# Performance work log

Hardware: AMD Instinct MI355X
Metric: run time of the kernel (lower is better)

The kernel has to match this reference:

```python
import jax, jax.numpy as jnp
import numpy as np

EMB = 1024
HEADS = 16
HEAD_DIM = EMB // HEADS


def setup_inputs() -> dict:
    key = jax.random.key(0)
    ks = jax.random.split(key, 11)
    B, S = 4, 2048
    scale = 1.0 / np.sqrt(EMB)
    inp = {
        "query": jax.random.normal(ks[0], (B, S, EMB), jnp.float32),
        "key": jax.random.normal(ks[1], (B, S, EMB), jnp.float32),
        "value": jax.random.normal(ks[2], (B, S, EMB), jnp.float32),
        "Wq": jax.random.normal(ks[3], (EMB, EMB), jnp.float32) * scale,
        "bq": jnp.zeros((EMB,), jnp.float32),
        "Wk": jax.random.normal(ks[4], (EMB, EMB), jnp.float32) * scale,
        "bk": jnp.zeros((EMB,), jnp.float32),
        "Wv": jax.random.normal(ks[5], (EMB, EMB), jnp.float32) * scale,
        "bv": jnp.zeros((EMB,), jnp.float32),
        "Wo": jax.random.normal(ks[6], (EMB, EMB), jnp.float32) * scale,
        "bo": jnp.zeros((EMB,), jnp.float32),
    }
    return inp


def reference(query, key, value, Wq, bq, Wk, bk, Wv, bv, Wo, bo):
    B, S, E = query.shape
    H, D = HEADS, HEAD_DIM

    def split_heads(x):  # [B,S,E] -> [B,H,S,D]
        return x.reshape(B, -1, H, D).transpose(0, 2, 1, 3)

    Q = split_heads(query @ Wq + bq)
    K = split_heads(key @ Wk + bk)
    V = split_heads(value @ Wv + bv)

    scores = jnp.einsum("bhqd,bhkd->bhqk", Q, K) / jnp.sqrt(jnp.float32(D))
    attn = jax.nn.softmax(scores, axis=-1)
    out = jnp.einsum("bhqk,bhkd->bhqd", attn, V)
    out = out.transpose(0, 2, 1, 3).reshape(B, S, E)
    return out @ Wo + bo
```

## Files before the change

kernel.cpp:

```cpp
#include <hip/hip_runtime.h>

typedef unsigned short ushort_t;
typedef __attribute__((ext_vector_type(8))) short bf16x8;
typedef __attribute__((ext_vector_type(4))) float f32x4;
typedef __attribute__((ext_vector_type(16))) float f32x16;
typedef __attribute__((ext_vector_type(4))) int i32x4;
typedef __attribute__((ext_vector_type(2))) unsigned int u32x2;

#define QSCALE 0.1803368801111204f

__device__ inline ushort_t f2bf(float f) {
    unsigned int u = __float_as_uint(f);
    unsigned int r = (u + 0x7FFFu + ((u >> 16) & 1u)) >> 16;
    return (ushort_t)r;
}
__device__ inline unsigned pkbf(float x, float y) {
    unsigned d;
    asm("v_cvt_pk_bf16_f32 %0, %1, %2" : "=v"(d) : "v"(x), "v"(y));
    return d;
}
__device__ inline float vexp2(float x) {
    float r;
    asm("v_exp_f32 %0, %1" : "=v"(r) : "v"(x));
    return r;
}
__device__ inline bf16x8 frag_from(unsigned a, unsigned b, unsigned c, unsigned d) {
    union { i32x4 i; bf16x8 v; } u;
    u.i[0] = (int)a; u.i[1] = (int)b; u.i[2] = (int)c; u.i[3] = (int)d;
    return u.v;
}

__device__ inline bf16x8 mkfrag(float x0, float x1, float x2, float x3,
                                float x4, float x5, float x6, float x7, int hi) {
    unsigned A_ = pkbf(x0, x1), B_ = pkbf(x2, x3), C_ = pkbf(x4, x5), D_ = pkbf(x6, x7);
    unsigned Ax = (unsigned)__shfl_xor((int)A_, 32);
    unsigned Bx = (unsigned)__shfl_xor((int)B_, 32);
    unsigned Cx = (unsigned)__shfl_xor((int)C_, 32);
    unsigned Dx = (unsigned)__shfl_xor((int)D_, 32);
    return frag_from(hi ? Cx : A_, hi ? Dx : B_, hi ? C_ : Ax, hi ? D_ : Bx);
}

__global__ __launch_bounds__(256) void transpose_cast4(
    const float* __restrict__ W0, const float* __restrict__ W1,
    const float* __restrict__ W2, const float* __restrict__ W3,
    ushort_t* __restrict__ T0, ushort_t* __restrict__ T1,
    ushort_t* __restrict__ T2, ushort_t* __restrict__ T3) {
    __shared__ float tile[32][33];
    const int which = blockIdx.x >> 10;
    const float* W = which == 0 ? W0 : which == 1 ? W1 : which == 2 ? W2 : W3;
    ushort_t* Wt = which == 0 ? T0 : which == 1 ? T1 : which == 2 ? T2 : T3;
    const int bidx = blockIdx.x & 1023;
    const int bx = bidx & 31, by = bidx >> 5;
    const int n0 = bx * 32, k0 = by * 32;
    const int tx = threadIdx.x & 31, ty = threadIdx.x >> 5;
#pragma unroll
    for (int i = 0; i < 4; ++i) {
        int r = ty + i * 8;
        tile[r][tx] = W[(k0 + r) * 1024 + n0 + tx];
    }
    __syncthreads();
#pragma unroll
    for (int i = 0; i < 4; ++i) {
        int r = ty + i * 8;
        Wt[(n0 + r) * 1024 + k0 + tx] = f2bf(tile[tx][r]);
    }
}

__global__ __launch_bounds__(256) void v_transpose(const ushort_t* __restrict__ Vp,
                                                   ushort_t* __restrict__ Vt) {
    __shared__ alignas(16) ushort_t tile[64][72];
    const int bid = blockIdx.x;
    const int pair = bid >> 5, st0 = (bid & 31) * 64;
    const ushort_t* src = Vp + (size_t)pair * 2048 * 64;
    ushort_t* dst = Vt + (size_t)pair * 64 * 2048;
    const int t = threadIdx.x;
    const int sl = t >> 2, d0 = (t & 3) * 16;
    *(bf16x8*)&tile[sl][d0] = *(const bf16x8*)&src[(size_t)(st0 + sl) * 64 + d0];
    *(bf16x8*)&tile[sl][d0 + 8] = *(const bf16x8*)&src[(size_t)(st0 + sl) * 64 + d0 + 8];
    __syncthreads();
    const int dl = t >> 2, s0 = (t & 3) * 16;
    bf16x8 a, b;
#pragma unroll
    for (int j = 0; j < 8; ++j) {
        a[j] = (short)tile[s0 + j][dl];
        b[j] = (short)tile[s0 + 8 + j][dl];
    }
    *(bf16x8*)&dst[(size_t)dl * 2048 + st0 + s0] = a;
    *(bf16x8*)&dst[(size_t)dl * 2048 + st0 + s0 + 8] = b;
}

template <int AF32, int OMODE>
__global__ __launch_bounds__(256) void gemm_bt(const void* __restrict__ Ap,
                                               const ushort_t* __restrict__ Bt,
                                               const float* __restrict__ bias,
                                               void* __restrict__ out, float scale) {
    constexpr int ASTR = AF32 ? 72 : 64;
    __shared__ alignas(16) ushort_t As[128 * ASTR];
    __shared__ alignas(16) ushort_t Bs[128 * 64];
    const int t = threadIdx.x;
    const int lane = t & 63, w = t >> 6;
    const int q = lane & 15, g = lane >> 4;
    const int wr = w >> 1, wc = w & 1;
    const int bm = blockIdx.x & 63, bn = blockIdx.x >> 6;
    const int m0 = bm * 128, n0 = bn * 128;

    const char* Btc = (const char*)Bt;
    char* AsB = (char*)As;
    char* BsB = (char*)Bs;

    f32x4 acc[4][4];
#pragma unroll
    for (int i = 0; i < 4; ++i)
#pragma unroll
        for (int j = 0; j < 4; ++j) acc[i][j] = (f32x4){0.f, 0.f, 0.f, 0.f};

    for (int k0 = 0; k0 < 1024; k0 += 64) {
        __syncthreads();
#pragma unroll
        for (int i = 0; i < 4; ++i) {
            const int c = w * 4 + i;
            __builtin_amdgcn_global_load_lds(
                (const __attribute__((address_space(1))) void*)(
                    Btc + (size_t)(n0 + c * 8 + (lane >> 3)) * 2048 + k0 * 2 + (lane & 7) * 16),
                (__attribute__((address_space(3))) void*)(BsB + c * 1024), 16, 0, 0);
        }
        if (AF32) {
            const float* A = (const float*)Ap;
#pragma unroll
            for (int it = 0; it < 4; ++it) {
                int tt = t + it * 256;
                int row = tt >> 3;
                int col = (tt & 7) * 8;
                float4 v0 = *(const float4*)&A[(size_t)(m0 + row) * 1024 + k0 + col];
                float4 v1 = *(const float4*)&A[(size_t)(m0 + row) * 1024 + k0 + col + 4];
                *(bf16x8*)&As[row * ASTR + col] =
                    frag_from(pkbf(v0.x, v0.y), pkbf(v0.z, v0.w),
                              pkbf(v1.x, v1.y), pkbf(v1.z, v1.w));
            }
        } else {
            const char* Ac = (const char*)Ap;
#pragma unroll
            for (int i = 0; i < 4; ++i) {
                const int c = w * 4 + i;
                __builtin_amdgcn_global_load_lds(
                    (const __attribute__((address_space(1))) void*)(
                        Ac + (size_t)(m0 + c * 8 + (lane >> 3)) * 2048 + k0 * 2 + (lane & 7) * 16),
                    (__attribute__((address_space(3))) void*)(AsB + c * 1024), 16, 0, 0);
            }
        }
        __syncthreads();
#pragma unroll
        for (int kt = 0; kt < 2; ++kt) {
            bf16x8 af[4], bfr[4];
#pragma unroll
            for (int mt = 0; mt < 4; ++mt)
                af[mt] = *(const bf16x8*)&As[(wr * 64 + mt * 16 + q) * ASTR + kt * 32 + g * 8];
#pragma unroll
            for (int nt = 0; nt < 4; ++nt)
                bfr[nt] = *(const bf16x8*)&Bs[(wc * 64 + nt * 16 + q) * 64 + kt * 32 + g * 8];
#pragma unroll
            for (int mt = 0; mt < 4; ++mt)
#pragma unroll
                for (int nt = 0; nt < 4; ++nt)
                    acc[mt][nt] = __builtin_amdgcn_mfma_f32_16x16x32_bf16(
                        af[mt], bfr[nt], acc[mt][nt], 0, 0, 0);
        }
    }

#pragma unroll
    for (int mt = 0; mt < 4; ++mt) {
#pragma unroll
        for (int nt = 0; nt < 4; ++nt) {
#pragma unroll
            for (int r = 0; r < 4; ++r) {
                int grow = m0 + wr * 64 + mt * 16 + g * 4 + r;
                int col = n0 + wc * 64 + nt * 16 + q;
                float v = acc[mt][nt][r] + bias[col];
                if (OMODE == 0) {
                    int b = grow >> 11, s = grow & 2047;
                    int h = col >> 6, d = col & 63;
                    ((ushort_t*)out)[(((size_t)(b * 16 + h) * 2048 + s) * 64) + d] =
                        f2bf(v * scale);
                } else {
                    ((float*)out)[(size_t)grow * 1024 + col] = v;
                }
            }
        }
    }
}

__global__ __launch_bounds__(512, 4) void attn_kernel(const ushort_t* __restrict__ Qp,
                                                      const ushort_t* __restrict__ Kp,
                                                      const ushort_t* __restrict__ Vtp,
                                                      ushort_t* __restrict__ Oa) {
    __shared__ alignas(16) ushort_t Ks[2][4096];
    __shared__ alignas(16) ushort_t Vs[2][4096];

    const int t = threadIdx.x, lane = t & 63, w = t >> 6;
    const int li = lane & 31, hi = lane >> 5;
    const int bid = (blockIdx.x & 7) * 64 + (blockIdx.x >> 3);
    const int pair = bid >> 3;
    const int qbase = (bid & 7) * 256 + w * 32;

    const ushort_t* Qh = Qp + (size_t)pair * 2048 * 64;
    const ushort_t* Kh = Kp + (size_t)pair * 2048 * 64;
    const ushort_t* Vh = Vtp + (size_t)pair * 64 * 2048;

    bf16x8 qf[4];
#pragma unroll
    for (int ks = 0; ks < 4; ++ks)
        qf[ks] = *(const bf16x8*)&Qh[(size_t)(qbase + li) * 64 + ks * 16 + hi * 8];

    const short one_bf = (short)0x3F80;
    const bf16x8 onesf = {one_bf, one_bf, one_bf, one_bf, one_bf, one_bf, one_bf, one_bf};
    const f32x16 z16 = {0.f,0.f,0.f,0.f,0.f,0.f,0.f,0.f,0.f,0.f,0.f,0.f,0.f,0.f,0.f,0.f};

    f32x16 o0 = z16, o1 = z16, osum = z16;
    float m_ = -1e30f;

    const int r8 = t >> 3;
    const int lcol = (t & 7) * 16;
    const int swoff = (r8 * 128) + (lcol ^ ((r8 & 7) << 4));
    const char* kp0 = (const char*)Kh + (size_t)r8 * 128 + lcol;
    const char* vp0 = (const char*)Vh + (size_t)r8 * 4096 + lcol;
    char* KsB = (char*)Ks;
    char* VsB = (char*)Vs;
    const int sw = (li & 7) << 4;

    i32x4 gk0 = *(const i32x4*)(kp0);
    i32x4 gv0 = *(const i32x4*)(vp0);
    *(i32x4*)(KsB + swoff) = gk0;
    *(i32x4*)(VsB + swoff) = gv0;
    gk0 = *(const i32x4*)(kp0 + 8192);
    gv0 = *(const i32x4*)(vp0 + 128);
    __syncthreads();

    for (int it = 0; it < 32; ++it) {
        const int cur = it & 1;
        if (it < 31) {
            const int nb = (cur ^ 1) * 8192;
            *(i32x4*)(KsB + nb + swoff) = gk0;
            *(i32x4*)(VsB + nb + swoff) = gv0;
        }
        if (it < 30) {
            gk0 = *(const i32x4*)(kp0 + (size_t)(it + 2) * 8192);
            gv0 = *(const i32x4*)(vp0 + (size_t)(it + 2) * 128);
        }

        const char* kb = KsB + cur * 8192;
        const char* vb = VsB + cur * 8192;

        f32x16 s0, s1;
        __builtin_amdgcn_s_setprio(1);
        {
            const int b = hi * 16;
            bf16x8 k0 = *(const bf16x8*)(kb + li * 128 + (b ^ sw));
            bf16x8 k1 = *(const bf16x8*)(kb + (32 + li) * 128 + (b ^ sw));
            s0 = __builtin_amdgcn_mfma_f32_32x32x16_bf16(k0, qf[0], z16, 0, 0, 0);
            s1 = __builtin_amdgcn_mfma_f32_32x32x16_bf16(k1, qf[0], z16, 0, 0, 0);
        }
#pragma unroll
        for (int ks = 1; ks < 4; ++ks) {
            const int b = ks * 32 + hi * 16;
            bf16x8 k0 = *(const bf16x8*)(kb + li * 128 + (b ^ sw));
            bf16x8 k1 = *(const bf16x8*)(kb + (32 + li) * 128 + (b ^ sw));
            s0 = __builtin_amdgcn_mfma_f32_32x32x16_bf16(k0, qf[ks], s0, 0, 0, 0);
            s1 = __builtin_amdgcn_mfma_f32_32x32x16_bf16(k1, qf[ks], s1, 0, 0, 0);
        }
        __builtin_amdgcn_s_setprio(0);

        float mx[8];
#pragma unroll
        for (int j = 0; j < 8; ++j)
            mx[j] = fmaxf(fmaxf(s0[j], s0[j + 8]), fmaxf(s1[j], s1[j + 8]));
        float m01 = fmaxf(mx[0], mx[1]), m23 = fmaxf(mx[2], mx[3]);
        float m45 = fmaxf(mx[4], mx[5]), m67 = fmaxf(mx[6], mx[7]);
        float tm = fmaxf(fmaxf(m01, m23), fmaxf(m45, m67));
        tm = fmaxf(tm, __shfl_xor(tm, 32));
        if (__any(tm > m_ + 8.f)) {
            float mn = fmaxf(m_, tm);
            float corr = vexp2(m_ - mn);
#pragma unroll
            for (int r = 0; r < 16; ++r) { o0[r] *= corr; o1[r] *= corr; }
            osum[0] *= corr;
            m_ = mn;
        }
#pragma unroll
        for (int r = 0; r < 16; ++r) s0[r] = vexp2(s0[r] - m_);
#pragma unroll
        for (int r = 0; r < 16; ++r) s1[r] = vexp2(s1[r] - m_);

        bf16x8 pf[4];
        pf[0] = mkfrag(s0[0], s0[1], s0[2], s0[3], s0[4], s0[5], s0[6], s0[7], hi);
        pf[1] = mkfrag(s0[8], s0[9], s0[10], s0[11], s0[12], s0[13], s0[14], s0[15], hi);
        pf[2] = mkfrag(s1[0], s1[1], s1[2], s1[3], s1[4], s1[5], s1[6], s1[7], hi);
        pf[3] = mkfrag(s1[8], s1[9], s1[10], s1[11], s1[12], s1[13], s1[14], s1[15], hi);

        __builtin_amdgcn_s_setprio(1);
#pragma unroll
        for (int ks = 0; ks < 4; ++ks) {
            const int b = ks * 32 + hi * 16;
            bf16x8 v0 = *(const bf16x8*)(vb + li * 128 + (b ^ sw));
            bf16x8 v1 = *(const bf16x8*)(vb + (32 + li) * 128 + (b ^ sw));
            o0 = __builtin_amdgcn_mfma_f32_32x32x16_bf16(v0, pf[ks], o0, 0, 0, 0);
            o1 = __builtin_amdgcn_mfma_f32_32x32x16_bf16(v1, pf[ks], o1, 0, 0, 0);
            osum = __builtin_amdgcn_mfma_f32_32x32x16_bf16(onesf, pf[ks], osum, 0, 0, 0);
        }
        __builtin_amdgcn_s_setprio(0);

        __syncthreads();
    }

    const float rl = 1.0f / osum[0];
    const int b = pair >> 4, hh = pair & 15;
    const int s = qbase + li;
    const size_t rowbase = ((size_t)(b * 2048 + s)) * 1024 + hh * 64;
#pragma unroll
    for (int dt = 0; dt < 2; ++dt) {
#pragma unroll
        for (int rq = 0; rq < 4; ++rq) {
            float v0 = (dt ? o1[rq * 4 + 0] : o0[rq * 4 + 0]) * rl;
            float v1 = (dt ? o1[rq * 4 + 1] : o0[rq * 4 + 1]) * rl;
            float v2 = (dt ? o1[rq * 4 + 2] : o0[rq * 4 + 2]) * rl;
            float v3 = (dt ? o1[rq * 4 + 3] : o0[rq * 4 + 3]) * rl;
            u32x2 uv;
            uv[0] = pkbf(v0, v1);
            uv[1] = pkbf(v2, v3);
            *(u32x2*)&Oa[rowbase + dt * 32 + rq * 8 + hi * 4] = uv;
        }
    }
}

extern "C" void kernel_launch(void* const* d_in, const int* in_sizes, int n_in,
                              void* d_out, int out_size, void* d_ws, size_t ws_size,
                              hipStream_t stream) {
    const float* query = (const float*)d_in[0];
    const float* key_ = (const float*)d_in[1];
    const float* value = (const float*)d_in[2];
    const float* Wq = (const float*)d_in[3];
    const float* bq = (const float*)d_in[4];
    const float* Wk = (const float*)d_in[5];
    const float* bk = (const float*)d_in[6];
    const float* Wv = (const float*)d_in[7];
    const float* bv = (const float*)d_in[8];
    const float* Wo = (const float*)d_in[9];
    const float* bo = (const float*)d_in[10];
    float* out = (float*)d_out;

    char* ws = (char*)d_ws;
    ushort_t* Wqt = (ushort_t*)(ws + 0);
    ushort_t* Wkt = (ushort_t*)(ws + 2097152);
    ushort_t* Wvt = (ushort_t*)(ws + 4194304);
    ushort_t* Wot = (ushort_t*)(ws + 6291456);
    ushort_t* Qp = (ushort_t*)(ws + 8388608);
    ushort_t* Kp = (ushort_t*)(ws + 25165824);
    ushort_t* Vp = (ushort_t*)(ws + 41943040);
    ushort_t* Vt = (ushort_t*)(ws + 58720256);
    ushort_t* Oa = (ushort_t*)(ws + 41943040);

    transpose_cast4<<<4096, 256, 0, stream>>>(Wq, Wk, Wv, Wo, Wqt, Wkt, Wvt, Wot);

    gemm_bt<1, 0><<<512, 256, 0, stream>>>((const void*)query, Wqt, bq, (void*)Qp, QSCALE);
    gemm_bt<1, 0><<<512, 256, 0, stream>>>((const void*)key_, Wkt, bk, (void*)Kp, 1.0f);
    gemm_bt<1, 0><<<512, 256, 0, stream>>>((const void*)value, Wvt, bv, (void*)Vp, 1.0f);

    v_transpose<<<2048, 256, 0, stream>>>(Vp, Vt);

    attn_kernel<<<512, 512, 0, stream>>>(Qp, Kp, Vt, Oa);

    gemm_bt<0, 1><<<512, 256, 0, stream>>>((const void*)Oa, Wot, bo, (void*)out, 1.0f);
}
```

Baseline: 244.1 us.

## Swizzle GEMM LDS tiles and compute softmax row sums with VALU instead of MFMA

The GEMM kernel now XOR-swizzles the 16-byte global source slots for global_load_lds and applies the same swizzle on LDS fragment reads. The goal is to remove LDS bank conflicts in the bf16 A and B tiles. The attention kernel drops the extra ones-matrix MFMA used for the row sum and instead adds the fp32 exponentials with VALU adds and one cross-half shuffle. This removes a third of the PV-stage MFMAs but adds about 16 adds per iteration, and the sum is now taken over fp32 values rather than the bf16-rounded ones.

```diff
diff --git a/kernel.cpp b/kernel.cpp
--- a/kernel.cpp
+++ b/kernel.cpp
@@ -107,6 +107,8 @@
     const char* Btc = (const char*)Bt;
     char* AsB = (char*)As;
     char* BsB = (char*)Bs;
+    const int grow8 = lane >> 3;
+    const int gslot = ((lane & 7) ^ (grow8 & 7)) << 4;
 
     f32x4 acc[4][4];
 #pragma unroll
@@ -121,7 +123,7 @@
             const int c = w * 4 + i;
             __builtin_amdgcn_global_load_lds(
                 (const __attribute__((address_space(1))) void*)(
-                    Btc + (size_t)(n0 + c * 8 + (lane >> 3)) * 2048 + k0 * 2 + (lane & 7) * 16),
+                    Btc + (size_t)(n0 + c * 8 + grow8) * 2048 + k0 * 2 + gslot),
                 (__attribute__((address_space(3))) void*)(BsB + c * 1024), 16, 0, 0);
         }
         if (AF32) {
@@ -144,7 +146,7 @@
                 const int c = w * 4 + i;
                 __builtin_amdgcn_global_load_lds(
                     (const __attribute__((address_space(1))) void*)(
-                        Ac + (size_t)(m0 + c * 8 + (lane >> 3)) * 2048 + k0 * 2 + (lane & 7) * 16),
+                        Ac + (size_t)(m0 + c * 8 + grow8) * 2048 + k0 * 2 + gslot),
                     (__attribute__((address_space(3))) void*)(AsB + c * 1024), 16, 0, 0);
             }
         }
@@ -153,11 +155,20 @@
         for (int kt = 0; kt < 2; ++kt) {
             bf16x8 af[4], bfr[4];
 #pragma unroll
-            for (int mt = 0; mt < 4; ++mt)
-                af[mt] = *(const bf16x8*)&As[(wr * 64 + mt * 16 + q) * ASTR + kt * 32 + g * 8];
-#pragma unroll
-            for (int nt = 0; nt < 4; ++nt)
-                bfr[nt] = *(const bf16x8*)&Bs[(wc * 64 + nt * 16 + q) * 64 + kt * 32 + g * 8];
+            for (int mt = 0; mt < 4; ++mt) {
+                const int row = wr * 64 + mt * 16 + q;
+                if (AF32)
+                    af[mt] = *(const bf16x8*)&As[row * 72 + kt * 32 + g * 8];
+                else
+                    af[mt] = *(const bf16x8*)(AsB + row * 128 +
+                                              (((kt * 4 + g) ^ (q & 7)) << 4));
+            }
+#pragma unroll
+            for (int nt = 0; nt < 4; ++nt) {
+                const int row = wc * 64 + nt * 16 + q;
+                bfr[nt] = *(const bf16x8*)(BsB + row * 128 +
+                                           (((kt * 4 + g) ^ (q & 7)) << 4));
+            }
 #pragma unroll
             for (int mt = 0; mt < 4; ++mt)
 #pragma unroll
@@ -211,12 +222,9 @@
     for (int ks = 0; ks < 4; ++ks)
         qf[ks] = *(const bf16x8*)&Qh[(size_t)(qbase + li) * 64 + ks * 16 + hi * 8];
 
-    const short one_bf = (short)0x3F80;
-    const bf16x8 onesf = {one_bf, one_bf, one_bf, one_bf, one_bf, one_bf, one_bf, one_bf};
     const f32x16 z16 = {0.f,0.f,0.f,0.f,0.f,0.f,0.f,0.f,0.f,0.f,0.f,0.f,0.f,0.f,0.f,0.f};
-
-    f32x16 o0 = z16, o1 = z16, osum = z16;
-    float m_ = -1e30f;
+    f32x16 o0 = z16, o1 = z16;
+    float m_ = -1e30f, l_ = 0.f;
 
     const int r8 = t >> 3;
     const int lcol = (t & 7) * 16;
@@ -282,13 +290,22 @@
             float corr = vexp2(m_ - mn);
 #pragma unroll
             for (int r = 0; r < 16; ++r) { o0[r] *= corr; o1[r] *= corr; }
-            osum[0] *= corr;
+            l_ *= corr;
             m_ = mn;
         }
 #pragma unroll
         for (int r = 0; r < 16; ++r) s0[r] = vexp2(s0[r] - m_);
 #pragma unroll
         for (int r = 0; r < 16; ++r) s1[r] = vexp2(s1[r] - m_);
+        float su[8];
+#pragma unroll
+        for (int j = 0; j < 8; ++j)
+            su[j] = (s0[j] + s0[j + 8]) + (s1[j] + s1[j + 8]);
+        float s01 = su[0] + su[1], s23 = su[2] + su[3];
+        float s45 = su[4] + su[5], s67 = su[6] + su[7];
+        float sum = (s01 + s23) + (s45 + s67);
+        sum += __shfl_xor(sum, 32);
+        l_ += sum;
 
         bf16x8 pf[4];
         pf[0] = mkfrag(s0[0], s0[1], s0[2], s0[3], s0[4], s0[5], s0[6], s0[7], hi);
@@ -304,14 +321,13 @@
             bf16x8 v1 = *(const bf16x8*)(vb + (32 + li) * 128 + (b ^ sw));
             o0 = __builtin_amdgcn_mfma_f32_32x32x16_bf16(v0, pf[ks], o0, 0, 0, 0);
             o1 = __builtin_amdgcn_mfma_f32_32x32x16_bf16(v1, pf[ks], o1, 0, 0, 0);
-            osum = __builtin_amdgcn_mfma_f32_32x32x16_bf16(onesf, pf[ks], osum, 0, 0, 0);
         }
         __builtin_amdgcn_s_setprio(0);
 
         __syncthreads();
     }
 
-    const float rl = 1.0f / osum[0];
+    const float rl = 1.0f / l_;
     const int b = pair >> 4, hh = pair & 15;
     const int s = qbase + li;
     const size_t rowbase = ((size_t)(b * 2048 + s)) * 1024 + hh * 64;
```

Result: faster. 229.0 us (-6.2%).
